# Optimization experiments

Measured on AMD Instinct MI355X. Metric: run time of the kernel, lower is better.

Reference implementation:

```python
import jax, jax.numpy as jnp
import numpy as np

B, S, D_IN, D_OUT, H = 4, 2048, 2048, 2048, 16
DH = D_OUT // H  # 128


def setup_inputs() -> dict:
    key = jax.random.key(0)
    ks = jax.random.split(key, 6)
    scale = 1.0 / np.sqrt(D_IN)
    return {
        "x": jax.random.normal(ks[0], (B, S, D_IN), dtype=jnp.float32),
        "Wq": jax.random.normal(ks[1], (D_IN, D_OUT), dtype=jnp.float32) * scale,
        "Wk": jax.random.normal(ks[2], (D_IN, D_OUT), dtype=jnp.float32) * scale,
        "Wv": jax.random.normal(ks[3], (D_IN, D_OUT), dtype=jnp.float32) * scale,
        "Wo": jax.random.normal(ks[4], (D_OUT, D_OUT), dtype=jnp.float32) * scale,
        "bo": jax.random.normal(ks[5], (D_OUT,), dtype=jnp.float32) * 0.01,
    }


def reference(x, Wq, Wk, Wv, Wo, bo):
    b, s, _ = x.shape
    # QKV projections (Linear, no bias), split into heads: [b, s, H, DH]
    q = (x @ Wq).reshape(b, s, H, DH)
    k = (x @ Wk).reshape(b, s, H, DH)
    v = (x @ Wv).reshape(b, s, H, DH)
    # attn_scores = Q @ K^T  -> [b, H, s, s]
    scores = jnp.einsum("bqhd,bkhd->bhqk", q, k)
    # causal mask: position q may only attend to k <= q
    causal = jnp.tril(jnp.ones((s, s), dtype=bool))
    scores = jnp.where(causal, scores, -jnp.inf)
    attn = jax.nn.softmax(scores / np.sqrt(DH).astype(np.float32), axis=-1)
    # dropout p = 0.0 -> identity
    ctx = jnp.einsum("bhqk,bkhd->bqhd", attn, v).reshape(b, s, D_OUT)
    return ctx @ Wo + bo
```

## Files before the change

kernel.cpp:

```cpp
#include <hip/hip_runtime.h>
#include <stdint.h>

typedef unsigned short u16;
typedef __attribute__((ext_vector_type(4))) float f32x4;
typedef __attribute__((ext_vector_type(8))) __bf16 bf16x8;
typedef __attribute__((address_space(3))) void lds_void;
typedef const __attribute__((address_space(1))) void gbl_void;

__device__ __forceinline__ u16 f2bf(float f) {
    uint32_t u = __float_as_uint(f);
    u += 0x7FFFu + ((u >> 16) & 1u);
    return (u16)(u >> 16);
}

__global__ __launch_bounds__(256) void cvt_bf16_kernel(const float* __restrict__ in,
                                                       u16* __restrict__ out, int n4) {
    int i = blockIdx.x * 256 + threadIdx.x;
    if (i >= n4) return;
    float4 v = reinterpret_cast<const float4*>(in)[i];
    ushort4 o;
    o.x = f2bf(v.x); o.y = f2bf(v.y); o.z = f2bf(v.z); o.w = f2bf(v.w);
    reinterpret_cast<ushort4*>(out)[i] = o;
}

__global__ __launch_bounds__(256) void transpose_w_kernel(const float* __restrict__ W,
                                                          u16* __restrict__ Wt) {
    __shared__ float tile[32][33];
    const int bx = blockIdx.x, by = blockIdx.y;
    const int tx = threadIdx.x;
    const int ty = threadIdx.y;
#pragma unroll
    for (int i = 0; i < 4; i++)
        tile[ty + i * 8][tx] = W[(size_t)(by * 32 + ty + i * 8) * 2048 + bx * 32 + tx];
    __syncthreads();
#pragma unroll
    for (int i = 0; i < 4; i++)
        Wt[(size_t)(bx * 32 + ty + i * 8) * 2048 + by * 32 + tx] = f2bf(tile[tx][ty + i * 8]);
}

template <bool F32OUT>
__global__ __launch_bounds__(256) void gemm_bt_kernel(const u16* __restrict__ A,
                                                      const u16* __restrict__ Bt,
                                                      void* __restrict__ Cout,
                                                      const float* __restrict__ bias,
                                                      int M, int N, int K) {
    __shared__ u16 As[128 * 32];
    __shared__ u16 Bs[128 * 32];
    const int tid = threadIdx.x;
    const int lane = tid & 63, wave = tid >> 6;
    const int l15 = lane & 15, l4 = lane >> 4;
    const int wm = wave >> 1, wn = wave & 1;
    const int bm = blockIdx.x, bn = blockIdx.y;

    f32x4 acc[4][4] = {};

    const int r0 = tid >> 2;
    const int r1 = r0 + 64;
    const int c0 = (tid & 3) * 8;
    const u16* ga0 = A + (size_t)(bm * 128 + r0) * K + c0;
    const u16* ga1 = A + (size_t)(bm * 128 + r1) * K + c0;
    const u16* gb0 = Bt + (size_t)(bn * 128 + r0) * K + c0;
    const u16* gb1 = Bt + (size_t)(bn * 128 + r1) * K + c0;
    const int ldsoff = wave * 1024;

    for (int kb = 0; kb < K; kb += 32) {
        __builtin_amdgcn_global_load_lds((gbl_void*)(ga0 + kb),
                                         (lds_void*)((char*)As + ldsoff), 16, 0, 0);
        __builtin_amdgcn_global_load_lds((gbl_void*)(ga1 + kb),
                                         (lds_void*)((char*)As + 4096 + ldsoff), 16, 0, 0);
        __builtin_amdgcn_global_load_lds((gbl_void*)(gb0 + kb),
                                         (lds_void*)((char*)Bs + ldsoff), 16, 0, 0);
        __builtin_amdgcn_global_load_lds((gbl_void*)(gb1 + kb),
                                         (lds_void*)((char*)Bs + 4096 + ldsoff), 16, 0, 0);
        __syncthreads();

        bf16x8 af[4], bfr[4];
#pragma unroll
        for (int m = 0; m < 4; ++m)
            af[m] = *reinterpret_cast<const bf16x8*>(&As[(wm * 64 + m * 16 + l15) * 32 + l4 * 8]);
#pragma unroll
        for (int n = 0; n < 4; ++n)
            bfr[n] = *reinterpret_cast<const bf16x8*>(&Bs[(wn * 64 + n * 16 + l15) * 32 + l4 * 8]);
#pragma unroll
        for (int m = 0; m < 4; ++m)
#pragma unroll
            for (int n = 0; n < 4; ++n)
                acc[m][n] = __builtin_amdgcn_mfma_f32_16x16x32_bf16(af[m], bfr[n], acc[m][n], 0, 0, 0);
        __syncthreads();
    }

    const int rbase = bm * 128 + wm * 64;
    const int cbase = bn * 128 + wn * 64;
#pragma unroll
    for (int m = 0; m < 4; ++m) {
#pragma unroll
        for (int n = 0; n < 4; ++n) {
            const int c = cbase + n * 16 + l15;
#pragma unroll
            for (int j = 0; j < 4; ++j) {
                const int r = rbase + m * 16 + l4 * 4 + j;
                if (F32OUT)
                    ((float*)Cout)[(size_t)r * N + c] = acc[m][n][j] + bias[c];
                else
                    ((u16*)Cout)[(size_t)r * N + c] = f2bf(acc[m][n][j]);
            }
        }
    }
}

__global__ __launch_bounds__(256) void attn_kernel(const u16* __restrict__ qk,
                                                   const u16* __restrict__ vt,
                                                   u16* __restrict__ ctx) {
    __shared__ u16 Ks[64 * 128];
    __shared__ u16 Vs[128 * 64];
    __shared__ u16 Ps[4 * 16 * 64];
    const int tid = threadIdx.x, lane = tid & 63, w = tid >> 6;
    const int l15 = lane & 15, l4 = lane >> 4;
    const int flat = blockIdx.x;
    const int qt = 31 - (flat >> 6);
    const int bh = flat & 63;
    const int b = bh >> 4, h = bh & 15;
    const int qb = qt * 64;

    bf16x8 qf[4];
    {
        const size_t rowQ = (size_t)(b * 2048 + qb + w * 16 + l15) * 4096 + h * 128;
#pragma unroll
        for (int kk = 0; kk < 4; kk++)
            qf[kk] = *reinterpret_cast<const bf16x8*>(&qk[rowQ + kk * 32 + l4 * 8]);
    }

    const int krow_i = tid >> 4, kslot = tid & 15;
    const int vrow_i = tid >> 3, vslot = tid & 7;

    float m_r[4], l_r[4];
    f32x4 o[8] = {};
#pragma unroll
    for (int j = 0; j < 4; ++j) { m_r[j] = -1e30f; l_r[j] = 0.f; }

    for (int kt = 0; kt <= qt; ++kt) {
        const int kvb = kt * 64;
#pragma unroll
        for (int p = 0; p < 4; ++p) {
            const int rowk = p * 16 + krow_i;
            const int ck = kslot ^ (rowk & 15);
            __builtin_amdgcn_global_load_lds(
                (gbl_void*)(qk + (size_t)(b * 2048 + kvb + rowk) * 4096 + 2048 + h * 128 + ck * 8),
                (lds_void*)((char*)Ks + p * 4096 + w * 1024), 16, 0, 0);
        }
#pragma unroll
        for (int p = 0; p < 4; ++p) {
            const int rowv = p * 32 + vrow_i;
            const int cv = vslot ^ (rowv & 7);
            __builtin_amdgcn_global_load_lds(
                (gbl_void*)(vt + (size_t)(h * 128 + rowv) * 8192 + b * 2048 + kvb + cv * 8),
                (lds_void*)((char*)Vs + p * 4096 + w * 1024), 16, 0, 0);
        }
        __syncthreads();

        f32x4 s[4] = {};
#pragma unroll
        for (int cb = 0; cb < 4; ++cb) {
            const int krow = cb * 16 + l15;
#pragma unroll
            for (int kk = 0; kk < 4; ++kk) {
                bf16x8 kf = *reinterpret_cast<const bf16x8*>(
                    &Ks[krow * 128 + (((kk * 4 + l4) ^ (krow & 15)) << 3)]);
                s[cb] = __builtin_amdgcn_mfma_f32_16x16x32_bf16(qf[kk], kf, s[cb], 0, 0, 0);
            }
        }
        const float sc = 0.08838834764831845f;
#pragma unroll
        for (int cb = 0; cb < 4; ++cb) s[cb] *= sc;

        if (kt == qt) {
#pragma unroll
            for (int cb = 0; cb < 4; ++cb)
#pragma unroll
                for (int j = 0; j < 4; ++j) {
                    int lr = w * 16 + l4 * 4 + j, lc = cb * 16 + l15;
                    if (lc > lr) s[cb][j] = -1e30f;
                }
        }

#pragma unroll
        for (int j = 0; j < 4; ++j) {
            float tm = fmaxf(fmaxf(s[0][j], s[1][j]), fmaxf(s[2][j], s[3][j]));
#pragma unroll
            for (int msk = 1; msk < 16; msk <<= 1)
                tm = fmaxf(tm, __shfl_xor(tm, msk, 64));
            float mnew = fmaxf(m_r[j], tm);
            float alpha = __expf(m_r[j] - mnew);
            m_r[j] = mnew;
            float rs = 0.f;
#pragma unroll
            for (int cb = 0; cb < 4; ++cb) {
                float p = __expf(s[cb][j] - mnew);
                s[cb][j] = p;
                rs += p;
            }
#pragma unroll
            for (int msk = 1; msk < 16; msk <<= 1)
                rs += __shfl_xor(rs, msk, 64);
            l_r[j] = l_r[j] * alpha + rs;
#pragma unroll
            for (int d = 0; d < 8; ++d) o[d][j] *= alpha;
        }

#pragma unroll
        for (int cb = 0; cb < 4; ++cb)
#pragma unroll
            for (int j = 0; j < 4; ++j) {
                const int r = l4 * 4 + j;
                const int e = cb * 16 + l15;
                Ps[w * 1024 + r * 64 + (((e >> 3) ^ (r & 7)) << 3) + (e & 7)] = f2bf(s[cb][j]);
            }

#pragma unroll
        for (int ks = 0; ks < 2; ++ks) {
            bf16x8 pf = *reinterpret_cast<const bf16x8*>(
                &Ps[w * 1024 + l15 * 64 + (((ks * 4 + l4) ^ (l15 & 7)) << 3)]);
#pragma unroll
            for (int d = 0; d < 8; ++d) {
                const int dr = d * 16 + l15;
                bf16x8 vf = *reinterpret_cast<const bf16x8*>(
                    &Vs[dr * 64 + (((ks * 4 + l4) ^ (dr & 7)) << 3)]);
                o[d] = __builtin_amdgcn_mfma_f32_16x16x32_bf16(pf, vf, o[d], 0, 0, 0);
            }
        }
        __syncthreads();
    }

#pragma unroll
    for (int j = 0; j < 4; ++j) {
        float inv = 1.0f / l_r[j];
        size_t row = (size_t)(b * 2048 + qb + w * 16 + l4 * 4 + j) * 2048 + h * 128;
#pragma unroll
        for (int d = 0; d < 8; ++d)
            ctx[row + d * 16 + l15] = f2bf(o[d][j] * inv);
    }
}

extern "C" void kernel_launch(void* const* d_in, const int* in_sizes, int n_in,
                              void* d_out, int out_size, void* d_ws, size_t ws_size,
                              hipStream_t stream) {
    const float* x  = (const float*)d_in[0];
    const float* Wq = (const float*)d_in[1];
    const float* Wk = (const float*)d_in[2];
    const float* Wv = (const float*)d_in[3];
    const float* Wo = (const float*)d_in[4];
    const float* bo = (const float*)d_in[5];
    float* out = (float*)d_out;

    char* ws = (char*)d_ws;
    u16* xb  = (u16*)(ws);
    u16* wt  = (u16*)(ws + 33554432);
    u16* wto = (u16*)(ws + 33554432 + 25165824);
    u16* qk  = (u16*)(ws + 67108864);
    u16* vtb = (u16*)(ws + 134217728);
    u16* wtv = wt + 2 * 2048 * 2048;
    u16* ctxb = xb;

    cvt_bf16_kernel<<<16384, 256, 0, stream>>>(x, xb, 4194304);
    dim3 tb(32, 8), tg(64, 64);
    transpose_w_kernel<<<tg, tb, 0, stream>>>(Wq, wt);
    transpose_w_kernel<<<tg, tb, 0, stream>>>(Wk, wt + 2048 * 2048);
    transpose_w_kernel<<<tg, tb, 0, stream>>>(Wv, wtv);
    transpose_w_kernel<<<tg, tb, 0, stream>>>(Wo, wto);

    gemm_bt_kernel<false><<<dim3(64, 32), 256, 0, stream>>>(xb, wt, qk, nullptr, 8192, 4096, 2048);
    gemm_bt_kernel<false><<<dim3(16, 64), 256, 0, stream>>>(wtv, xb, vtb, nullptr, 2048, 8192, 2048);
    attn_kernel<<<2048, 256, 0, stream>>>(qk, vtb, ctxb);
    gemm_bt_kernel<true><<<dim3(64, 16), 256, 0, stream>>>(ctxb, wto, out, bo, 8192, 2048, 2048);
}
```

Before: 600.7 us.

## Triple-buffer GEMM LDS tiles with async prefetch and XCD-aware block remap

The GEMM main loop now keeps three LDS stages and issues global-to-LDS loads two tiles ahead, using explicit vmcnt waits and raw barriers in place of the load-then-sync pattern. This hides global load latency behind the MFMA work. It also remaps the workgroup index so consecutive tiles land on the same XCD, which should improve L2 reuse. LDS use triples to 48KB per block, which may lower occupancy.

```diff
diff --git a/kernel.cpp b/kernel.cpp
--- a/kernel.cpp
+++ b/kernel.cpp
@@ -44,13 +44,20 @@
                                                       void* __restrict__ Cout,
                                                       const float* __restrict__ bias,
                                                       int M, int N, int K) {
-    __shared__ u16 As[128 * 32];
-    __shared__ u16 Bs[128 * 32];
+    __shared__ u16 As[3 * 4096];
+    __shared__ u16 Bs[3 * 4096];
     const int tid = threadIdx.x;
     const int lane = tid & 63, wave = tid >> 6;
     const int l15 = lane & 15, l4 = lane >> 4;
     const int wm = wave >> 1, wn = wave & 1;
-    const int bm = blockIdx.x, bn = blockIdx.y;
+
+    const int gx = gridDim.x;
+    const int nwg = gx * gridDim.y;
+    const int flat0 = blockIdx.y * gx + blockIdx.x;
+    const int q = nwg >> 3, r = nwg & 7;
+    const int xcd = flat0 & 7, idx = flat0 >> 3;
+    const int wgid = (xcd < r ? xcd * (q + 1) : r * (q + 1) + (xcd - r) * q) + idx;
+    const int bm = wgid % gx, bn = wgid / gx;
 
     f32x4 acc[4][4] = {};
 
@@ -61,33 +68,60 @@
     const u16* ga1 = A + (size_t)(bm * 128 + r1) * K + c0;
     const u16* gb0 = Bt + (size_t)(bn * 128 + r0) * K + c0;
     const u16* gb1 = Bt + (size_t)(bn * 128 + r1) * K + c0;
-    const int ldsoff = wave * 1024;
-
-    for (int kb = 0; kb < K; kb += 32) {
-        __builtin_amdgcn_global_load_lds((gbl_void*)(ga0 + kb),
-                                         (lds_void*)((char*)As + ldsoff), 16, 0, 0);
-        __builtin_amdgcn_global_load_lds((gbl_void*)(ga1 + kb),
-                                         (lds_void*)((char*)As + 4096 + ldsoff), 16, 0, 0);
-        __builtin_amdgcn_global_load_lds((gbl_void*)(gb0 + kb),
-                                         (lds_void*)((char*)Bs + ldsoff), 16, 0, 0);
-        __builtin_amdgcn_global_load_lds((gbl_void*)(gb1 + kb),
-                                         (lds_void*)((char*)Bs + 4096 + ldsoff), 16, 0, 0);
-        __syncthreads();
-
+    const int woff = wave * 1024;
+
+#define STAGE_TILE(T, SLOT)                                                              \
+    {                                                                                    \
+        const int kb_ = (T) << 5;                                                        \
+        const int sb_ = (SLOT) * 8192;                                                   \
+        __builtin_amdgcn_global_load_lds((gbl_void*)(ga0 + kb_),                         \
+                                         (lds_void*)((char*)As + sb_ + woff), 16, 0, 0); \
+        __builtin_amdgcn_global_load_lds((gbl_void*)(ga1 + kb_),                         \
+                                         (lds_void*)((char*)As + sb_ + 4096 + woff), 16, 0, 0); \
+        __builtin_amdgcn_global_load_lds((gbl_void*)(gb0 + kb_),                         \
+                                         (lds_void*)((char*)Bs + sb_ + woff), 16, 0, 0); \
+        __builtin_amdgcn_global_load_lds((gbl_void*)(gb1 + kb_),                         \
+                                         (lds_void*)((char*)Bs + sb_ + 4096 + woff), 16, 0, 0); \
+    }
+
+    const int nt = K >> 5;
+    STAGE_TILE(0, 0);
+    STAGE_TILE(1, 1);
+
+    int cs = 0, ps = 2;
+    for (int t = 0; t < nt; ++t) {
+        if (t + 2 < nt) {
+            STAGE_TILE(t + 2, ps);
+            asm volatile("s_waitcnt vmcnt(8)" ::: "memory");
+        } else if (t + 2 == nt) {
+            asm volatile("s_waitcnt vmcnt(4)" ::: "memory");
+        } else {
+            asm volatile("s_waitcnt vmcnt(0)" ::: "memory");
+        }
+        __builtin_amdgcn_s_barrier();
+        __builtin_amdgcn_sched_barrier(0);
+
+        const u16* as = As + cs * 4096;
+        const u16* bs = Bs + cs * 4096;
         bf16x8 af[4], bfr[4];
 #pragma unroll
         for (int m = 0; m < 4; ++m)
-            af[m] = *reinterpret_cast<const bf16x8*>(&As[(wm * 64 + m * 16 + l15) * 32 + l4 * 8]);
+            af[m] = *reinterpret_cast<const bf16x8*>(&as[(wm * 64 + m * 16 + l15) * 32 + l4 * 8]);
 #pragma unroll
         for (int n = 0; n < 4; ++n)
-            bfr[n] = *reinterpret_cast<const bf16x8*>(&Bs[(wn * 64 + n * 16 + l15) * 32 + l4 * 8]);
+            bfr[n] = *reinterpret_cast<const bf16x8*>(&bs[(wn * 64 + n * 16 + l15) * 32 + l4 * 8]);
 #pragma unroll
         for (int m = 0; m < 4; ++m)
 #pragma unroll
             for (int n = 0; n < 4; ++n)
                 acc[m][n] = __builtin_amdgcn_mfma_f32_16x16x32_bf16(af[m], bfr[n], acc[m][n], 0, 0, 0);
-        __syncthreads();
-    }
+
+        __builtin_amdgcn_s_barrier();
+        __builtin_amdgcn_sched_barrier(0);
+        cs = (cs == 2) ? 0 : cs + 1;
+        ps = (ps == 2) ? 0 : ps + 1;
+    }
+#undef STAGE_TILE
 
     const int rbase = bm * 128 + wm * 64;
     const int cbase = bn * 128 + wn * 64;
@@ -98,11 +132,11 @@
             const int c = cbase + n * 16 + l15;
 #pragma unroll
             for (int j = 0; j < 4; ++j) {
-                const int r = rbase + m * 16 + l4 * 4 + j;
+                const int rr = rbase + m * 16 + l4 * 4 + j;
                 if (F32OUT)
-                    ((float*)Cout)[(size_t)r * N + c] = acc[m][n][j] + bias[c];
+                    ((float*)Cout)[(size_t)rr * N + c] = acc[m][n][j] + bias[c];
                 else
-                    ((u16*)Cout)[(size_t)r * N + c] = f2bf(acc[m][n][j]);
+                    ((u16*)Cout)[(size_t)rr * N + c] = f2bf(acc[m][n][j]);
             }
         }
     }
@@ -211,9 +245,9 @@
         for (int cb = 0; cb < 4; ++cb)
 #pragma unroll
             for (int j = 0; j < 4; ++j) {
-                const int r = l4 * 4 + j;
+                const int rr = l4 * 4 + j;
                 const int e = cb * 16 + l15;
-                Ps[w * 1024 + r * 64 + (((e >> 3) ^ (r & 7)) << 3) + (e & 7)] = f2bf(s[cb][j]);
+                Ps[w * 1024 + rr * 64 + (((e >> 3) ^ (rr & 7)) << 3) + (e & 7)] = f2bf(s[cb][j]);
             }
 
 #pragma unroll
```

Measured after the change: 590.2 us. No clear change (-1.7%).

## Replace GEMM with 256x256 double-buffered tiled kernel using swizzled LDS

Applied to the files above, without the earlier changes.

Replaces the 128x128, K=32 single-buffered GEMM with a 256x256-tile, 512-thread kernel. It double-buffers 64-wide K slices in 128KB of LDS, using an XOR swizzle to avoid bank conflicts. Loads for the next tile are issued in four quarter-phases interleaved with MFMA work, with setprio around the MFMA bursts, so global latency overlaps compute and per-tile barrier stalls shrink. The larger tile raises data reuse but increases register and LDS pressure and leaves fewer blocks in each grid.

```diff
diff --git a/kernel.cpp b/kernel.cpp
--- a/kernel.cpp
+++ b/kernel.cpp
@@ -39,70 +39,114 @@
 }
 
 template <bool F32OUT>
-__global__ __launch_bounds__(256) void gemm_bt_kernel(const u16* __restrict__ A,
-                                                      const u16* __restrict__ Bt,
-                                                      void* __restrict__ Cout,
-                                                      const float* __restrict__ bias,
-                                                      int M, int N, int K) {
-    __shared__ u16 As[128 * 32];
-    __shared__ u16 Bs[128 * 32];
+__global__ __launch_bounds__(512, 2) void gemm256_kernel(const u16* __restrict__ A,
+                                                         const u16* __restrict__ Bt,
+                                                         void* __restrict__ Cout,
+                                                         const float* __restrict__ bias,
+                                                         int M, int N, int K) {
+    __shared__ u16 lds[65536];
     const int tid = threadIdx.x;
-    const int lane = tid & 63, wave = tid >> 6;
+    const int lane = tid & 63, w = tid >> 6;
     const int l15 = lane & 15, l4 = lane >> 4;
-    const int wm = wave >> 1, wn = wave & 1;
+    const int wm = w >> 2, wn = w & 3;
     const int bm = blockIdx.x, bn = blockIdx.y;
 
-    f32x4 acc[4][4] = {};
-
-    const int r0 = tid >> 2;
-    const int r1 = r0 + 64;
-    const int c0 = (tid & 3) * 8;
-    const u16* ga0 = A + (size_t)(bm * 128 + r0) * K + c0;
-    const u16* ga1 = A + (size_t)(bm * 128 + r1) * K + c0;
-    const u16* gb0 = Bt + (size_t)(bn * 128 + r0) * K + c0;
-    const u16* gb1 = Bt + (size_t)(bn * 128 + r1) * K + c0;
-    const int ldsoff = wave * 1024;
-
-    for (int kb = 0; kb < K; kb += 32) {
-        __builtin_amdgcn_global_load_lds((gbl_void*)(ga0 + kb),
-                                         (lds_void*)((char*)As + ldsoff), 16, 0, 0);
-        __builtin_amdgcn_global_load_lds((gbl_void*)(ga1 + kb),
-                                         (lds_void*)((char*)As + 4096 + ldsoff), 16, 0, 0);
-        __builtin_amdgcn_global_load_lds((gbl_void*)(gb0 + kb),
-                                         (lds_void*)((char*)Bs + ldsoff), 16, 0, 0);
-        __builtin_amdgcn_global_load_lds((gbl_void*)(gb1 + kb),
-                                         (lds_void*)((char*)Bs + 4096 + ldsoff), 16, 0, 0);
-        __syncthreads();
-
-        bf16x8 af[4], bfr[4];
-#pragma unroll
-        for (int m = 0; m < 4; ++m)
-            af[m] = *reinterpret_cast<const bf16x8*>(&As[(wm * 64 + m * 16 + l15) * 32 + l4 * 8]);
-#pragma unroll
-        for (int n = 0; n < 4; ++n)
-            bfr[n] = *reinterpret_cast<const bf16x8*>(&Bs[(wn * 64 + n * 16 + l15) * 32 + l4 * 8]);
-#pragma unroll
-        for (int m = 0; m < 4; ++m)
-#pragma unroll
-            for (int n = 0; n < 4; ++n)
-                acc[m][n] = __builtin_amdgcn_mfma_f32_16x16x32_bf16(af[m], bfr[n], acc[m][n], 0, 0, 0);
-        __syncthreads();
-    }
-
-    const int rbase = bm * 128 + wm * 64;
-    const int cbase = bn * 128 + wn * 64;
-#pragma unroll
-    for (int m = 0; m < 4; ++m) {
-#pragma unroll
-        for (int n = 0; n < 4; ++n) {
-            const int c = cbase + n * 16 + l15;
+    f32x4 acc[8][4] = {};
+
+    const int srow = tid >> 3;
+    const int scs = (tid & 7) ^ (srow & 7);
+    const u16* gA = A + (size_t)(bm * 256 + srow) * K + scs * 8;
+    const u16* gB = Bt + (size_t)(bn * 256 + srow) * K + scs * 8;
+    const size_t rowK64 = (size_t)64 * K;
+    u16* ldst = lds + tid * 8;
+
+#define STAGE_HALF(D, OP, H, T)                                                           \
+    {                                                                                     \
+        const u16* g_ = ((OP) ? gB : gA) + (size_t)(H) * 128 * K + (size_t)(T) * 64;      \
+        u16* l_ = ldst + (D) * 32768 + (OP) * 16384 + (H) * 8192;                         \
+        __builtin_amdgcn_global_load_lds((gbl_void*)g_, (lds_void*)l_, 16, 0, 0);         \
+        __builtin_amdgcn_global_load_lds((gbl_void*)(g_ + rowK64), (lds_void*)(l_ + 4096),\
+                                         16, 0, 0);                                       \
+    }
+
+#define PHASE(D, Q, T1, ST, GEND)                                                         \
+    {                                                                                     \
+        const int mh = (Q) >> 1, nh = (Q) & 1;                                            \
+        bf16x8 af[4][2], bfr[2][2];                                                       \
+        const u16* ab = lds + (D) * 32768 + wm * 8192;                                    \
+        const u16* bb = lds + (D) * 32768 + 16384 + (wn >> 1) * 8192;                     \
+        _Pragma("unroll") for (int mm = 0; mm < 4; ++mm) {                                \
+            const int ra = mh * 64 + mm * 16 + l15;                                       \
+            _Pragma("unroll") for (int kk = 0; kk < 2; ++kk)                              \
+                af[mm][kk] = *reinterpret_cast<const bf16x8*>(                            \
+                    &ab[ra * 64 + (((kk * 4 + l4) ^ (ra & 7)) << 3)]);                    \
+        }                                                                                 \
+        _Pragma("unroll") for (int nn = 0; nn < 2; ++nn) {                                \
+            const int rb = (wn & 1) * 64 + nh * 32 + nn * 16 + l15;                       \
+            _Pragma("unroll") for (int kk = 0; kk < 2; ++kk)                              \
+                bfr[nn][kk] = *reinterpret_cast<const bf16x8*>(                           \
+                    &bb[rb * 64 + (((kk * 4 + l4) ^ (rb & 7)) << 3)]);                    \
+        }                                                                                 \
+        if (ST) STAGE_HALF((D) ^ 1, ((Q) >> 1), ((Q) & 1), T1);                           \
+        __builtin_amdgcn_s_barrier();                                                     \
+        asm volatile("s_waitcnt lgkmcnt(0)" ::: "memory");                                \
+        __builtin_amdgcn_sched_barrier(0);                                                \
+        __builtin_amdgcn_s_setprio(1);                                                    \
+        _Pragma("unroll") for (int kk = 0; kk < 2; ++kk)                                  \
+            _Pragma("unroll") for (int mm = 0; mm < 4; ++mm)                              \
+                _Pragma("unroll") for (int nn = 0; nn < 2; ++nn)                          \
+                    acc[mh * 4 + mm][nh * 2 + nn] =                                       \
+                        __builtin_amdgcn_mfma_f32_16x16x32_bf16(                          \
+                            af[mm][kk], bfr[nn][kk], acc[mh * 4 + mm][nh * 2 + nn],       \
+                            0, 0, 0);                                                     \
+        __builtin_amdgcn_s_setprio(0);                                                    \
+        if (GEND) {                                                                       \
+            asm volatile("s_waitcnt vmcnt(0)" ::: "memory");                              \
+            __builtin_amdgcn_sched_barrier(0);                                            \
+        }                                                                                 \
+        __builtin_amdgcn_s_barrier();                                                     \
+    }
+
+    const int nt = K >> 6;
+    STAGE_HALF(0, 0, 0, 0);
+    STAGE_HALF(0, 0, 1, 0);
+    STAGE_HALF(0, 1, 0, 0);
+    STAGE_HALF(0, 1, 1, 0);
+    asm volatile("s_waitcnt vmcnt(0)" ::: "memory");
+    __builtin_amdgcn_sched_barrier(0);
+    __builtin_amdgcn_s_barrier();
+
+    for (int T = 0; T < nt; ++T) {
+        const bool st = (T + 1 < nt);
+        if ((T & 1) == 0) {
+            PHASE(0, 0, T + 1, st, false);
+            PHASE(0, 1, T + 1, st, false);
+            PHASE(0, 2, T + 1, st, false);
+            PHASE(0, 3, T + 1, st, true);
+        } else {
+            PHASE(1, 0, T + 1, st, false);
+            PHASE(1, 1, T + 1, st, false);
+            PHASE(1, 2, T + 1, st, false);
+            PHASE(1, 3, T + 1, st, true);
+        }
+    }
+#undef PHASE
+#undef STAGE_HALF
+
+    const int rbase = bm * 256 + wm * 128;
+    const int cbase = bn * 256 + wn * 64;
+#pragma unroll
+    for (int mi = 0; mi < 8; ++mi) {
+#pragma unroll
+        for (int ni = 0; ni < 4; ++ni) {
+            const int c = cbase + ni * 16 + l15;
 #pragma unroll
             for (int j = 0; j < 4; ++j) {
-                const int r = rbase + m * 16 + l4 * 4 + j;
+                const int rr = rbase + mi * 16 + l4 * 4 + j;
                 if (F32OUT)
-                    ((float*)Cout)[(size_t)r * N + c] = acc[m][n][j] + bias[c];
+                    ((float*)Cout)[(size_t)rr * N + c] = acc[mi][ni][j] + bias[c];
                 else
-                    ((u16*)Cout)[(size_t)r * N + c] = f2bf(acc[m][n][j]);
+                    ((u16*)Cout)[(size_t)rr * N + c] = f2bf(acc[mi][ni][j]);
             }
         }
     }
@@ -211,9 +255,9 @@
         for (int cb = 0; cb < 4; ++cb)
 #pragma unroll
             for (int j = 0; j < 4; ++j) {
-                const int r = l4 * 4 + j;
+                const int rr = l4 * 4 + j;
                 const int e = cb * 16 + l15;
-                Ps[w * 1024 + r * 64 + (((e >> 3) ^ (r & 7)) << 3) + (e & 7)] = f2bf(s[cb][j]);
+                Ps[w * 1024 + rr * 64 + (((e >> 3) ^ (rr & 7)) << 3) + (e & 7)] = f2bf(s[cb][j]);
             }
 
 #pragma unroll
@@ -268,8 +312,8 @@
     transpose_w_kernel<<<tg, tb, 0, stream>>>(Wv, wtv);
     transpose_w_kernel<<<tg, tb, 0, stream>>>(Wo, wto);
 
-    gemm_bt_kernel<false><<<dim3(64, 32), 256, 0, stream>>>(xb, wt, qk, nullptr, 8192, 4096, 2048);
-    gemm_bt_kernel<false><<<dim3(16, 64), 256, 0, stream>>>(wtv, xb, vtb, nullptr, 2048, 8192, 2048);
+    gemm256_kernel<false><<<dim3(32, 16), 512, 0, stream>>>(xb, wt, qk, nullptr, 8192, 4096, 2048);
+    gemm256_kernel<false><<<dim3(8, 32), 512, 0, stream>>>(wtv, xb, vtb, nullptr, 2048, 8192, 2048);
     attn_kernel<<<2048, 256, 0, stream>>>(qk, vtb, ctxb);
-    gemm_bt_kernel<true><<<dim3(64, 16), 256, 0, stream>>>(ctxb, wto, out, bo, 8192, 2048, 2048);
-}
+    gemm256_kernel<true><<<dim3(32, 8), 512, 0, stream>>>(ctxb, wto, out, bo, 8192, 2048, 2048);
+}
```

After: 1.492 ms. 2.48x slower.
